# Kernel tuning notes

Hardware: AMD Instinct MI355X
Metric: run time of the kernel (lower is better)

## Reference

```python
import jax, jax.numpy as jnp
import numpy as np

NEG_SLOPE = 0.2


def _gatv2_head(x, src, dst, W_l, W_r, att, bias, n_nodes):
    # x: [N, din]; src/dst: [E'] (self-loops already appended)
    xl = x @ W_l                      # [N, dout] source transform (messages)
    xr = x @ W_r                      # [N, dout] destination transform
    h = xl[src] + xr[dst]             # [E', dout] edge-wise gather
    e = jax.nn.leaky_relu(h, NEG_SLOPE) @ att   # [E'] attention logits
    # numerically stable per-destination softmax over ragged neighborhoods
    e_max = jax.ops.segment_max(e, dst, num_segments=n_nodes)   # [N]
    e_exp = jnp.exp(e - e_max[dst])                               # [E']
    denom = jax.ops.segment_sum(e_exp, dst, num_segments=n_nodes)  # [N]
    alpha = e_exp / denom[dst]                                     # [E']
    out = jax.ops.segment_sum(alpha[:, None] * xl[src], dst, num_segments=n_nodes)
    return out + bias                 # [N, dout]


def setup_inputs() -> dict:
    key = jax.random.key(0)
    H, N, E, DIN, DOUT = 4, 50000, 1600000, 32, 32
    ks = jax.random.split(key, 6)
    x = jax.random.normal(ks[0], (H, N, DIN), dtype=jnp.float32)
    edge_index = jax.random.randint(ks[1], (H, 2, E), 0, N, dtype=jnp.int64)
    W_l = jax.random.normal(ks[2], (H, DIN, DOUT), dtype=jnp.float32) / np.sqrt(DIN)
    W_r = jax.random.normal(ks[3], (H, DIN, DOUT), dtype=jnp.float32) / np.sqrt(DIN)
    att = jax.random.normal(ks[4], (H, DOUT), dtype=jnp.float32) / np.sqrt(DOUT)
    bias = jax.random.normal(ks[5], (H, DOUT), dtype=jnp.float32) * 0.01
    return {"x": x, "edge_index": edge_index, "W_l": W_l, "W_r": W_r,
            "att": att, "bias": bias}


def reference(x, edge_index, W_l, W_r, att, bias):
    H, N, _ = x.shape
    loops = jnp.arange(N, dtype=edge_index.dtype)

    def per_head(xh, eih, Wl, Wr, a, b):
        # add self-loops (PyG GATv2Conv default add_self_loops=True)
        src = jnp.concatenate([eih[0], loops])
        dst = jnp.concatenate([eih[1], loops])
        return _gatv2_head(xh, src, dst, Wl, Wr, a, b, N)

    out = jax.vmap(per_head)(x, edge_index, W_l, W_r, att, bias)  # [H, N, dout]
    # torch.cat(outputs, dim=-1): interleave heads last -> [N, H*dout]
    return jnp.transpose(out, (1, 0, 2)).reshape(N, -1)
```

## Files before the change

### kernel.cpp

```cpp
#include <hip/hip_runtime.h>

#define NEG_SLOPE 0.2f

static constexpr int Hh   = 4;
static constexpr int Nn   = 50000;
static constexpr int Ee   = 1600000;
static constexpr int D    = 32;

static constexpr int GBITS = 8;
static constexpr int GW    = 1 << GBITS;
static constexpr int BPH   = (Nn + GW - 1) / GW;
static constexpr int NBIN  = Hh * BPH;
static constexpr int CAP   = 9728;
static constexpr int T1    = 8192;
static constexpr int TPB1  = 512;
static constexpr int EPT   = T1 / TPB1;
static constexpr int NPT   = (Ee + T1 - 1) / T1;
static constexpr int NPB   = NPT * Hh;
static constexpr int NGRP  = Nn / 16;
static constexpr int TPART = 250;
static constexpr int NTB   = Hh * TPART;

typedef _Float16 v2h __attribute__((ext_vector_type(2)));
struct H8 { v2h a, b, c, d; };
union U16B { uint4 u; H8 h; };

#if defined(__has_builtin)
#if __has_builtin(__builtin_amdgcn_fdot2)
#define HAS_FDOT2 1
#endif
#endif

union SMem {
    struct {
        unsigned stage[T1];
        int lcur[BPH];
        int lstart[BPH];
        int gdst[BPH];
        int hs[256];
    } p;
    struct {
        float wl[D * D];
        float wr[D * D];
        float xs[16 * D];
    } t;
};

__global__ __launch_bounds__(TPB1)
void pass1_kernel(const float* __restrict__ x, const float* __restrict__ Wl,
                  const float* __restrict__ Wr, const int* __restrict__ ei,
                  _Float16* __restrict__ xlh, _Float16* __restrict__ xrh,
                  int* __restrict__ bincur, unsigned* __restrict__ seg1) {
    __shared__ SMem sm;
    const int L   = blockIdx.x;
    const int tid = threadIdx.x;

    if (L < NPB) {
        const int h  = L & 3;
        const int tb = (L >> 2) * T1;

        for (int i = tid; i < BPH; i += TPB1) sm.p.lcur[i] = 0;
        __syncthreads();

        const int4* srcp = (const int4*)(ei + (size_t)h * 2 * Ee);
        const int4* dstp = (const int4*)(ei + (size_t)h * 2 * Ee + Ee);

        unsigned ent[EPT];
        unsigned short rk[EPT];
#pragma unroll
        for (int k = 0; k < EPT / 4; ++k) {
            const int e4 = tb + 4 * (k * TPB1 + tid);
            if (e4 < Ee) {
                const int4 s4 = srcp[e4 >> 2];
                const int4 d4 = dstp[e4 >> 2];
                ent[4 * k + 0] = ((unsigned)s4.x << 16) | (unsigned)d4.x;
                ent[4 * k + 1] = ((unsigned)s4.y << 16) | (unsigned)d4.y;
                ent[4 * k + 2] = ((unsigned)s4.z << 16) | (unsigned)d4.z;
                ent[4 * k + 3] = ((unsigned)s4.w << 16) | (unsigned)d4.w;
                rk[4 * k + 0] = (unsigned short)atomicAdd(&sm.p.lcur[d4.x >> GBITS], 1);
                rk[4 * k + 1] = (unsigned short)atomicAdd(&sm.p.lcur[d4.y >> GBITS], 1);
                rk[4 * k + 2] = (unsigned short)atomicAdd(&sm.p.lcur[d4.z >> GBITS], 1);
                rk[4 * k + 3] = (unsigned short)atomicAdd(&sm.p.lcur[d4.w >> GBITS], 1);
            } else {
                ent[4*k+0] = ent[4*k+1] = ent[4*k+2] = ent[4*k+3] = 0xffffffffu;
            }
        }
        __syncthreads();

        if (tid < 256) sm.p.hs[tid] = (tid < BPH) ? sm.p.lcur[tid] : 0;
        __syncthreads();
        for (int o = 1; o < 256; o <<= 1) {
            int v = 0;
            if (tid < 256 && tid >= o) v = sm.p.hs[tid - o];
            __syncthreads();
            if (tid < 256) sm.p.hs[tid] += v;
            __syncthreads();
        }
        if (tid < BPH) {
            sm.p.lstart[tid] = sm.p.hs[tid] - sm.p.lcur[tid];
            if (sm.p.lcur[tid] > 0) {
                const int g = atomicAdd(&bincur[h * BPH + tid], sm.p.lcur[tid]);
                sm.p.gdst[tid] = (h * BPH + tid) * CAP + g;
            }
        }
        __syncthreads();

#pragma unroll
        for (int k = 0; k < EPT; ++k) {
            if (ent[k] != 0xffffffffu) {
                const int b = (int)((ent[k] & 0xffffu) >> GBITS);
                sm.p.stage[sm.p.lstart[b] + (int)rk[k]] = ent[k];
            }
        }
        __syncthreads();

        const int tot = sm.p.lstart[BPH - 1] + sm.p.lcur[BPH - 1];
        for (int i = tid; i < tot; i += TPB1) {
            const unsigned e = sm.p.stage[i];
            const int b = (int)((e & 0xffffu) >> GBITS);
            seg1[(size_t)sm.p.gdst[b] + (i - sm.p.lstart[b])] = e;
        }
    } else {
        const int t    = L - NPB;
        const int h    = t & 3;
        const int part = t >> 2;

        for (int i = tid; i < D * D; i += TPB1) {
            sm.t.wl[i] = Wl[h * D * D + i];
            sm.t.wr[i] = Wr[h * D * D + i];
        }

        const int node16 = tid >> 5;
        const int c      = tid & 31;

        for (int nb = part; nb < NGRP; nb += TPART) {
            __syncthreads();
            if (tid < 128) {
                const float4* xsrc =
                    (const float4*)(x + ((size_t)h * Nn + (size_t)nb * 16) * D);
                ((float4*)sm.t.xs)[tid] = xsrc[tid];
            }
            __syncthreads();

            const float* xrow = sm.t.xs + node16 * D;
            float al = 0.f, ar = 0.f;
#pragma unroll
            for (int k = 0; k < D; ++k) {
                const float xv = xrow[k];
                al = fmaf(xv, sm.t.wl[k * D + c], al);
                ar = fmaf(xv, sm.t.wr[k * D + c], ar);
            }
            const size_t o = ((size_t)h * Nn + (size_t)nb * 16 + node16) * D + c;
            xlh[o] = (_Float16)al;
            xrh[o] = (_Float16)ar;
        }
    }
}

__global__ __launch_bounds__(512)
void sortaccum_kernel(const int* __restrict__ bincur, const unsigned* __restrict__ seg1,
                      const _Float16* __restrict__ xlh, const _Float16* __restrict__ xrh,
                      const float* __restrict__ att, const float* __restrict__ bias,
                      float* __restrict__ out) {
    __shared__ int rcnt[GW];
    __shared__ int rcur[GW];
    __shared__ int rowbeg[GW + 1];
    __shared__ unsigned short s2[CAP];
    __shared__ unsigned short order[GW];
    __shared__ int nextrow;

    const int tid = threadIdx.x;
    const int L   = blockIdx.x;
    const int xcd = L & 7;
    const int h   = xcd >> 1;
    const int b   = ((L >> 3) << 1) | (L & 1);
    const int bin = h * BPH + b;
    const int nodebase = b * GW;
    const int nrows = (Nn - nodebase) < GW ? (Nn - nodebase) : GW;
    const int cnt   = bincur[bin];
    const size_t base = (size_t)bin * CAP;
    const int hbase = h * Nn;

    if (tid < GW) rcnt[tid] = 0;
    if (tid == 0) nextrow = 0;
    __syncthreads();

    for (int i = tid; i < cnt; i += 512)
        atomicAdd(&rcnt[seg1[base + i] & 0xffu], 1);
    __syncthreads();

    int v = 0;
    if (tid < GW) v = rcnt[tid];
    for (int o = 1; o < GW; o <<= 1) {
        int a = 0;
        if (tid < GW && tid >= o) a = rcnt[tid - o];
        __syncthreads();
        if (tid < GW) rcnt[tid] += a;
        __syncthreads();
    }
    if (tid < GW) {
        const int excl = rcnt[tid] - v;
        rcur[tid]   = excl;
        rowbeg[tid] = excl;
        if (tid == GW - 1) rowbeg[GW] = excl + v;
    }
    __syncthreads();

    for (int i = tid; i < cnt; i += 512) {
        const unsigned e = seg1[base + i];
        const int p = atomicAdd(&rcur[e & 0xffu], 1);
        s2[p] = (unsigned short)(e >> 16);
    }
    __syncthreads();

    if (tid < GW) rcnt[tid] = 0;
    __syncthreads();
    int key = 0;
    if (tid < nrows) {
        const int deg = rowbeg[tid + 1] - rowbeg[tid];
        key = deg > 255 ? 0 : 255 - deg;
        atomicAdd(&rcnt[key], 1);
    }
    __syncthreads();
    int kv = 0;
    if (tid < GW) kv = rcnt[tid];
    for (int o = 1; o < GW; o <<= 1) {
        int a = 0;
        if (tid < GW && tid >= o) a = rcnt[tid - o];
        __syncthreads();
        if (tid < GW) rcnt[tid] += a;
        __syncthreads();
    }
    if (tid < GW) rcur[tid] = rcnt[tid] - kv;
    __syncthreads();
    if (tid < nrows) {
        const int p = atomicAdd(&rcur[key], 1);
        order[p] = (unsigned short)tid;
    }
    __syncthreads();

    const int l4 = tid & 3;

    v2h a0, a1, a2, a3;
    {
        const float* ap = att + h * D + l4 * 8;
        a0[0] = (_Float16)ap[0]; a0[1] = (_Float16)ap[1];
        a1[0] = (_Float16)ap[2]; a1[1] = (_Float16)ap[3];
        a2[0] = (_Float16)ap[4]; a2[1] = (_Float16)ap[5];
        a3[0] = (_Float16)ap[6]; a3[1] = (_Float16)ap[7];
    }
    const v2h sl2 = {(_Float16)NEG_SLOPE, (_Float16)NEG_SLOPE};
    const float* bp = bias + h * D + l4 * 8;

    for (;;) {
        int t0 = 0;
        if (l4 == 0) t0 = atomicAdd(&nextrow, 1);
        const int q = __shfl(t0, 0, 4);
        if (q >= nrows) break;
        const int j = (int)order[q];

        const int n = nodebase + j;
        const int r = hbase + n;

        U16B xr8; xr8.u = *(const uint4*)(xrh + (size_t)r * D + l4 * 8);

        float ac0 = 0.f, ac1 = 0.f, ac2 = 0.f, ac3 = 0.f;
        float ac4 = 0.f, ac5 = 0.f, ac6 = 0.f, ac7 = 0.f;
        float den = 0.f;

        auto proc = [&](const H8& xg) {
            const v2h h0 = xg.a + xr8.h.a, h1 = xg.b + xr8.h.b;
            const v2h h2 = xg.c + xr8.h.c, h3 = xg.d + xr8.h.d;
            const v2h l0 = __builtin_elementwise_max(h0, h0 * sl2);
            const v2h l1 = __builtin_elementwise_max(h1, h1 * sl2);
            const v2h l2 = __builtin_elementwise_max(h2, h2 * sl2);
            const v2h l3 = __builtin_elementwise_max(h3, h3 * sl2);
            float p;
#ifdef HAS_FDOT2
            p = __builtin_amdgcn_fdot2(l0, a0, 0.f, false);
            p = __builtin_amdgcn_fdot2(l1, a1, p, false);
            p = __builtin_amdgcn_fdot2(l2, a2, p, false);
            p = __builtin_amdgcn_fdot2(l3, a3, p, false);
#else
            p  = (float)l0[0] * (float)a0[0] + (float)l0[1] * (float)a0[1];
            p += (float)l1[0] * (float)a1[0] + (float)l1[1] * (float)a1[1];
            p += (float)l2[0] * (float)a2[0] + (float)l2[1] * (float)a2[1];
            p += (float)l3[0] * (float)a3[0] + (float)l3[1] * (float)a3[1];
#endif
            p += __shfl_xor(p, 1, 4);
            p += __shfl_xor(p, 2, 4);
            const float w = __expf(p);
            ac0 = fmaf(w, (float)xg.a[0], ac0);
            ac1 = fmaf(w, (float)xg.a[1], ac1);
            ac2 = fmaf(w, (float)xg.b[0], ac2);
            ac3 = fmaf(w, (float)xg.b[1], ac3);
            ac4 = fmaf(w, (float)xg.c[0], ac4);
            ac5 = fmaf(w, (float)xg.c[1], ac5);
            ac6 = fmaf(w, (float)xg.d[0], ac6);
            ac7 = fmaf(w, (float)xg.d[1], ac7);
            den += w;
        };

        {
            U16B xs; xs.u = *(const uint4*)(xlh + (size_t)r * D + l4 * 8);
            proc(xs.h);
        }

        const int beg = rowbeg[j];
        const int end = rowbeg[j + 1];
        int jj = beg;
        for (; jj + 4 <= end; jj += 4) {
            const int sv = (int)s2[jj + l4];
#pragma unroll
            for (int k = 0; k < 4; ++k) {
                const int s = __shfl(sv, k, 4);
                U16B xg; xg.u = *(const uint4*)(xlh + (size_t)(hbase + s) * D + l4 * 8);
                proc(xg.h);
            }
        }
        if (jj < end) {
            const int m = end - jj;
            int idx = jj + l4;
            if (idx >= end) idx = end - 1;
            const int sv = (int)s2[idx];
            for (int k = 0; k < m; ++k) {
                const int s = __shfl(sv, k, 4);
                U16B xg; xg.u = *(const uint4*)(xlh + (size_t)(hbase + s) * D + l4 * 8);
                proc(xg.h);
            }
        }

        const float inv = 1.f / den;
        float* op = out + (size_t)n * (Hh * D) + h * D + l4 * 8;
        float4 o0, o1;
        o0.x = ac0 * inv + bp[0]; o0.y = ac1 * inv + bp[1];
        o0.z = ac2 * inv + bp[2]; o0.w = ac3 * inv + bp[3];
        o1.x = ac4 * inv + bp[4]; o1.y = ac5 * inv + bp[5];
        o1.z = ac6 * inv + bp[6]; o1.w = ac7 * inv + bp[7];
        ((float4*)op)[0] = o0;
        ((float4*)op)[1] = o1;
    }
}

extern "C" void kernel_launch(void* const* d_in, const int* in_sizes, int n_in,
                              void* d_out, int out_size, void* d_ws, size_t ws_size,
                              hipStream_t stream) {
    const float* x    = (const float*)d_in[0];
    const int*   ei   = (const int*)d_in[1];
    const float* Wl   = (const float*)d_in[2];
    const float* Wr   = (const float*)d_in[3];
    const float* att  = (const float*)d_in[4];
    const float* bias = (const float*)d_in[5];
    float* out = (float*)d_out;

    _Float16* xlh  = (_Float16*)d_ws;
    _Float16* xrh  = xlh + (size_t)Hh * Nn * D;
    unsigned* seg1 = (unsigned*)(xrh + (size_t)Hh * Nn * D);
    int*      bincur = (int*)(seg1 + (size_t)NBIN * CAP);

    hipMemsetAsync(bincur, 0, NBIN * sizeof(int), stream);

    pass1_kernel<<<NPB + NTB, TPB1, 0, stream>>>(x, Wl, Wr, ei, xlh, xrh, bincur, seg1);

    sortaccum_kernel<<<NBIN, 512, 0, stream>>>(bincur, seg1, xlh, xrh, att, bias, out);
}
```

Baseline: 224.7 us.

## Halve destination bin width and use static row assignment in accumulate kernel

Shrinks the destination bin width from 256 to 128 nodes, which doubles the number of bins (BPH padded to 392) and halves per-bin capacity and shared memory. The sortaccum kernel gets an occupancy hint and returns early for padded bins. It replaces the atomic dynamic row scheduler with a static stride over degree-sorted rows. The gather loop is rewritten to issue all four neighbor loads before processing them, exposing memory-level parallelism. The risks are more work-imbalance without dynamic scheduling and possible overflow of the smaller per-bin capacity.

```diff
diff --git a/kernel.cpp b/kernel.cpp
--- a/kernel.cpp
+++ b/kernel.cpp
@@ -7,11 +7,11 @@
 static constexpr int Ee   = 1600000;
 static constexpr int D    = 32;
 
-static constexpr int GBITS = 8;
+static constexpr int GBITS = 7;
 static constexpr int GW    = 1 << GBITS;
-static constexpr int BPH   = (Nn + GW - 1) / GW;
+static constexpr int BPH   = 392;
 static constexpr int NBIN  = Hh * BPH;
-static constexpr int CAP   = 9728;
+static constexpr int CAP   = 4864;
 static constexpr int T1    = 8192;
 static constexpr int TPB1  = 512;
 static constexpr int EPT   = T1 / TPB1;
@@ -37,7 +37,7 @@
         int lcur[BPH];
         int lstart[BPH];
         int gdst[BPH];
-        int hs[256];
+        int hs[512];
     } p;
     struct {
         float wl[D * D];
@@ -87,13 +87,13 @@
         }
         __syncthreads();
 
-        if (tid < 256) sm.p.hs[tid] = (tid < BPH) ? sm.p.lcur[tid] : 0;
-        __syncthreads();
-        for (int o = 1; o < 256; o <<= 1) {
+        sm.p.hs[tid] = (tid < BPH) ? sm.p.lcur[tid] : 0;
+        __syncthreads();
+        for (int o = 1; o < 512; o <<= 1) {
             int v = 0;
-            if (tid < 256 && tid >= o) v = sm.p.hs[tid - o];
+            if (tid >= o) v = sm.p.hs[tid - o];
             __syncthreads();
-            if (tid < 256) sm.p.hs[tid] += v;
+            sm.p.hs[tid] += v;
             __syncthreads();
         }
         if (tid < BPH) {
@@ -157,7 +157,7 @@
     }
 }
 
-__global__ __launch_bounds__(512)
+__global__ __launch_bounds__(512, 8)
 void sortaccum_kernel(const int* __restrict__ bincur, const unsigned* __restrict__ seg1,
                       const _Float16* __restrict__ xlh, const _Float16* __restrict__ xrh,
                       const float* __restrict__ att, const float* __restrict__ bias,
@@ -167,26 +167,25 @@
     __shared__ int rowbeg[GW + 1];
     __shared__ unsigned short s2[CAP];
     __shared__ unsigned short order[GW];
-    __shared__ int nextrow;
 
     const int tid = threadIdx.x;
     const int L   = blockIdx.x;
     const int xcd = L & 7;
     const int h   = xcd >> 1;
     const int b   = ((L >> 3) << 1) | (L & 1);
+    const int nodebase = b * GW;
+    if (nodebase >= Nn) return;
     const int bin = h * BPH + b;
-    const int nodebase = b * GW;
     const int nrows = (Nn - nodebase) < GW ? (Nn - nodebase) : GW;
     const int cnt   = bincur[bin];
     const size_t base = (size_t)bin * CAP;
     const int hbase = h * Nn;
 
     if (tid < GW) rcnt[tid] = 0;
-    if (tid == 0) nextrow = 0;
     __syncthreads();
 
     for (int i = tid; i < cnt; i += 512)
-        atomicAdd(&rcnt[seg1[base + i] & 0xffu], 1);
+        atomicAdd(&rcnt[seg1[base + i] & (GW - 1)], 1);
     __syncthreads();
 
     int v = 0;
@@ -208,7 +207,7 @@
 
     for (int i = tid; i < cnt; i += 512) {
         const unsigned e = seg1[base + i];
-        const int p = atomicAdd(&rcur[e & 0xffu], 1);
+        const int p = atomicAdd(&rcur[e & (GW - 1)], 1);
         s2[p] = (unsigned short)(e >> 16);
     }
     __syncthreads();
@@ -218,7 +217,7 @@
     int key = 0;
     if (tid < nrows) {
         const int deg = rowbeg[tid + 1] - rowbeg[tid];
-        key = deg > 255 ? 0 : 255 - deg;
+        key = deg > (GW - 1) ? 0 : (GW - 1 - deg);
         atomicAdd(&rcnt[key], 1);
     }
     __syncthreads();
@@ -239,7 +238,8 @@
     }
     __syncthreads();
 
-    const int l4 = tid & 3;
+    const int l4  = tid & 3;
+    const int gid = tid >> 2;
 
     v2h a0, a1, a2, a3;
     {
@@ -252,11 +252,7 @@
     const v2h sl2 = {(_Float16)NEG_SLOPE, (_Float16)NEG_SLOPE};
     const float* bp = bias + h * D + l4 * 8;
 
-    for (;;) {
-        int t0 = 0;
-        if (l4 == 0) t0 = atomicAdd(&nextrow, 1);
-        const int q = __shfl(t0, 0, 4);
-        if (q >= nrows) break;
+    for (int q = gid; q < nrows; q += 128) {
         const int j = (int)order[q];
 
         const int n = nodebase + j;
@@ -311,12 +307,19 @@
         int jj = beg;
         for (; jj + 4 <= end; jj += 4) {
             const int sv = (int)s2[jj + l4];
-#pragma unroll
-            for (int k = 0; k < 4; ++k) {
-                const int s = __shfl(sv, k, 4);
-                U16B xg; xg.u = *(const uint4*)(xlh + (size_t)(hbase + s) * D + l4 * 8);
-                proc(xg.h);
-            }
+            const int sa = __shfl(sv, 0, 4);
+            const int sb = __shfl(sv, 1, 4);
+            const int sc = __shfl(sv, 2, 4);
+            const int sd = __shfl(sv, 3, 4);
+            U16B g0, g1, g2, g3;
+            g0.u = *(const uint4*)(xlh + (size_t)(hbase + sa) * D + l4 * 8);
+            g1.u = *(const uint4*)(xlh + (size_t)(hbase + sb) * D + l4 * 8);
+            g2.u = *(const uint4*)(xlh + (size_t)(hbase + sc) * D + l4 * 8);
+            g3.u = *(const uint4*)(xlh + (size_t)(hbase + sd) * D + l4 * 8);
+            proc(g0.h);
+            proc(g1.h);
+            proc(g2.h);
+            proc(g3.h);
         }
         if (jj < end) {
             const int m = end - jj;
```

New measurement: 210.1 us. 1.07x faster.
